# Performance work log

Measured on AMD Instinct MI355X. Metric: run time of the kernel, lower is better.

The kernel has to match this reference:

```python
import jax, jax.numpy as jnp
import numpy as np

B, S, DIM, H = 8, 1024, 1024, 16
D = DIM // H  # d_head = 64


def setup_inputs() -> dict:
    key = jax.random.key(0)
    ks = jax.random.split(key, 7)
    scale = 1.0 / np.sqrt(D)  # nn.Linear default init range ~ U(-1/sqrt(in), 1/sqrt(in))
    x = jax.random.normal(ks[0], (B, S, DIM), dtype=jnp.float32)
    Wq = jax.random.uniform(ks[1], (H, D, D), jnp.float32, -scale, scale)
    Wk = jax.random.uniform(ks[2], (H, D, D), jnp.float32, -scale, scale)
    Wv = jax.random.uniform(ks[3], (H, D, D), jnp.float32, -scale, scale)
    bq = jax.random.uniform(ks[4], (H, D), jnp.float32, -scale, scale)
    bk = jax.random.uniform(ks[5], (H, D), jnp.float32, -scale, scale)
    bv = jax.random.uniform(ks[6], (H, D), jnp.float32, -scale, scale)
    return {"x": x, "Wq": Wq, "Wk": Wk, "Wv": Wv, "bq": bq, "bk": bk, "bv": bv}


def reference(x, Wq, Wk, Wv, bq, bk, bv):
    # x: [B,S,DIM] -> split heads: [B,S,H,D] (matches per-head column slicing)
    xh = x.reshape(x.shape[0], x.shape[1], H, D)
    # per-head linear: y = x @ W.T + b  (nn.Linear convention: weight [out,in])
    q = jnp.einsum('bshd,hed->bshe', xh, Wq) + bq  # [B,S,H,D]
    k = jnp.einsum('bshd,hed->bshe', xh, Wk) + bk
    v = jnp.einsum('bshd,hed->bshe', xh, Wv) + bv
    scores = jnp.einsum('bqhd,bkhd->bhqk', q, k) / jnp.sqrt(jnp.float32(D))
    attn = jax.nn.softmax(scores, axis=-1)  # [B,H,S,S]
    out = jnp.einsum('bhqk,bkhd->bqhd', attn, v)  # [B,S,H,D]
    # hstack over heads == merge last two dims back to DIM
    return out.reshape(x.shape[0], x.shape[1], H * D)
```

## Files before the change

kernel.cpp:

```cpp
#include <hip/hip_runtime.h>
#include <hip/hip_bf16.h>

#define BB 8
#define SS 1024
#define HH 16
#define DD 64
#define DIMM 1024
#define NUNITS (BB * HH)
#define UNIT_ELEMS (SS * DD)

typedef __attribute__((ext_vector_type(8))) short short8;
typedef __attribute__((ext_vector_type(4))) float f32x4;

__device__ inline short f2b(float f) {
    __hip_bfloat16 h = __float2bfloat16(f);
    return *reinterpret_cast<short*>(&h);
}

__global__ __launch_bounds__(256) void qkv_proj(
    const float* __restrict__ x, const float* __restrict__ Wq,
    const float* __restrict__ Wk, const float* __restrict__ Wv,
    const float* __restrict__ bqp, const float* __restrict__ bkp,
    const float* __restrict__ bvp,
    short* __restrict__ Qo, short* __restrict__ Ko, short* __restrict__ Vto,
    int unit0)
{
    __shared__ alignas(16) short xs[64][72];
    __shared__ alignas(16) short wsm[3][64][72];
    __shared__ alignas(16) short tr[64][72];

    const int t = threadIdx.x;
    const int bid = blockIdx.x;
    const int st = bid & 15;
    const int ul = bid >> 4;
    const int unit = unit0 + ul;
    const int h = unit & 15;
    const int b = unit >> 4;
    const int s0 = st * 64;

    for (int i = 0; i < 4; ++i) {
        int g = t + i * 256;
        int r = g >> 4, c = (g & 15) * 4;
        float4 xv = *reinterpret_cast<const float4*>(
            x + ((size_t)(b * SS + s0 + r)) * DIMM + h * DD + c);
        short4 sv; sv.x = f2b(xv.x); sv.y = f2b(xv.y); sv.z = f2b(xv.z); sv.w = f2b(xv.w);
        *reinterpret_cast<short4*>(&xs[r][c]) = sv;
    }
    {
        const float* Wsrc[3] = {Wq + h * DD * DD, Wk + h * DD * DD, Wv + h * DD * DD};
        for (int m = 0; m < 3; ++m)
            for (int i = 0; i < 4; ++i) {
                int g = t + i * 256;
                int e = g >> 4, c = (g & 15) * 4;
                float4 wv = *reinterpret_cast<const float4*>(Wsrc[m] + e * DD + c);
                short4 sv; sv.x = f2b(wv.x); sv.y = f2b(wv.y); sv.z = f2b(wv.z); sv.w = f2b(wv.w);
                *reinterpret_cast<short4*>(&wsm[m][e][c]) = sv;
            }
    }
    __syncthreads();

    const int lane = t & 63, w = t >> 6;
    const int l15 = lane & 15, quad = lane >> 4;

    short8 a0 = *reinterpret_cast<const short8*>(&xs[w * 16 + l15][quad * 8]);
    short8 a1 = *reinterpret_cast<const short8*>(&xs[w * 16 + l15][32 + quad * 8]);

    const float* biases[3] = {bqp, bkp, bvp};

    for (int m = 0; m < 3; ++m) {
        for (int et = 0; et < 4; ++et) {
            short8 w0 = *reinterpret_cast<const short8*>(&wsm[m][et * 16 + l15][quad * 8]);
            short8 w1 = *reinterpret_cast<const short8*>(&wsm[m][et * 16 + l15][32 + quad * 8]);
            f32x4 acc = {0.f, 0.f, 0.f, 0.f};
            acc = __builtin_amdgcn_mfma_f32_16x16x32_bf16(a0, w0, acc, 0, 0, 0);
            acc = __builtin_amdgcn_mfma_f32_16x16x32_bf16(a1, w1, acc, 0, 0, 0);
            float bias = biases[m][h * DD + et * 16 + l15];
            for (int r = 0; r < 4; ++r) {
                float v = acc[r] + bias;
                int e = et * 16 + l15;
                int srow = w * 16 + quad * 4 + r;
                if (m == 0) {
                    tr[srow][e] = f2b(v * 0.125f);
                } else if (m == 1) {
                    tr[srow][e] = f2b(v);
                } else {
                    tr[e][srow] = f2b(v);
                }
            }
        }
        __syncthreads();
        for (int i = 0; i < 2; ++i) {
            int g = t + i * 256;
            int row = g >> 3, col = (g & 7) * 8;
            short8 val = *reinterpret_cast<const short8*>(&tr[row][col]);
            if (m == 0)
                *reinterpret_cast<short8*>(Qo + ((size_t)ul * SS + s0 + row) * DD + col) = val;
            else if (m == 1)
                *reinterpret_cast<short8*>(Ko + ((size_t)ul * SS + s0 + row) * DD + col) = val;
            else
                *reinterpret_cast<short8*>(Vto + ((size_t)ul * DD + row) * SS + s0 + col) = val;
        }
        __syncthreads();
    }
}

__global__ __launch_bounds__(256, 4) void attn(
    const short* __restrict__ Q, const short* __restrict__ K,
    const short* __restrict__ Vt, float* __restrict__ out, int unit0)
{
    __shared__ alignas(16) short ks[64][72];
    __shared__ alignas(16) short vts[64][72];
    __shared__ alignas(16) short ps[4][32][72];

    const int t = threadIdx.x;
    const int bid = blockIdx.x;
    const int qt = bid & 7;
    const int ul = bid >> 3;
    const int unit = unit0 + ul;
    const int h = unit & 15;
    const int b = unit >> 4;
    const int q0 = qt * 128;
    const int lane = t & 63, w = t >> 6;
    const int l15 = lane & 15, quad = lane >> 4;

    short8 qa[2][2];
    for (int s = 0; s < 2; ++s) {
        const short* qp = Q + ((size_t)ul * SS + q0 + s * 64 + w * 16 + l15) * DD;
        qa[s][0] = *reinterpret_cast<const short8*>(qp + quad * 8);
        qa[s][1] = *reinterpret_cast<const short8*>(qp + 32 + quad * 8);
    }

    short8 ones;
    for (int j = 0; j < 8; ++j) ones[j] = (short)0x3F80;

    f32x4 o[8];
    f32x4 lacc[2];
    for (int i = 0; i < 8; ++i) o[i] = (f32x4){0.f, 0.f, 0.f, 0.f};
    lacc[0] = (f32x4){0.f, 0.f, 0.f, 0.f};
    lacc[1] = (f32x4){0.f, 0.f, 0.f, 0.f};

    const int srow_ = t >> 3, scol = (t & 7) * 8;

    const float L2E = 1.44269504f;
    const float MBIAS = 11.5415603f;

    for (int kt = 0; kt < 16; ++kt) {
        const int k0 = kt * 64;
        __syncthreads();
        for (int i = 0; i < 2; ++i) {
            int row = srow_ + i * 32;
            *reinterpret_cast<short8*>(&ks[row][scol]) =
                *reinterpret_cast<const short8*>(K + ((size_t)ul * SS + k0 + row) * DD + scol);
            *reinterpret_cast<short8*>(&vts[row][scol]) =
                *reinterpret_cast<const short8*>(Vt + ((size_t)ul * DD + row) * SS + k0 + scol);
        }
        __syncthreads();

        for (int n = 0; n < 4; ++n) {
            short8 kb0 = *reinterpret_cast<const short8*>(&ks[n * 16 + l15][quad * 8]);
            short8 kb1 = *reinterpret_cast<const short8*>(&ks[n * 16 + l15][32 + quad * 8]);
            for (int s = 0; s < 2; ++s) {
                f32x4 acc = {0.f, 0.f, 0.f, 0.f};
                acc = __builtin_amdgcn_mfma_f32_16x16x32_bf16(qa[s][0], kb0, acc, 0, 0, 0);
                acc = __builtin_amdgcn_mfma_f32_16x16x32_bf16(qa[s][1], kb1, acc, 0, 0, 0);
                for (int r = 0; r < 4; ++r) {
                    float p = exp2f(fmaf(acc[r], L2E, -MBIAS));
                    ps[w][s * 16 + quad * 4 + r][n * 16 + l15] = f2b(p);
                }
            }
        }

        short8 pa[2][2];
        for (int s = 0; s < 2; ++s) {
            pa[s][0] = *reinterpret_cast<const short8*>(&ps[w][s * 16 + l15][quad * 8]);
            pa[s][1] = *reinterpret_cast<const short8*>(&ps[w][s * 16 + l15][32 + quad * 8]);
            lacc[s] = __builtin_amdgcn_mfma_f32_16x16x32_bf16(pa[s][0], ones, lacc[s], 0, 0, 0);
            lacc[s] = __builtin_amdgcn_mfma_f32_16x16x32_bf16(pa[s][1], ones, lacc[s], 0, 0, 0);
        }
        for (int dt = 0; dt < 4; ++dt) {
            short8 vb0 = *reinterpret_cast<const short8*>(&vts[dt * 16 + l15][quad * 8]);
            short8 vb1 = *reinterpret_cast<const short8*>(&vts[dt * 16 + l15][32 + quad * 8]);
            for (int s = 0; s < 2; ++s) {
                o[s * 4 + dt] = __builtin_amdgcn_mfma_f32_16x16x32_bf16(pa[s][0], vb0, o[s * 4 + dt], 0, 0, 0);
                o[s * 4 + dt] = __builtin_amdgcn_mfma_f32_16x16x32_bf16(pa[s][1], vb1, o[s * 4 + dt], 0, 0, 0);
            }
        }
    }

    for (int s = 0; s < 2; ++s)
        for (int dt = 0; dt < 4; ++dt)
            for (int r = 0; r < 4; ++r) {
                int srow = q0 + s * 64 + w * 16 + quad * 4 + r;
                int col = h * DD + dt * 16 + l15;
                out[((size_t)b * SS + srow) * DIMM + col] = o[s * 4 + dt][r] / lacc[s][r];
            }
}

extern "C" void kernel_launch(void* const* d_in, const int* in_sizes, int n_in,
                              void* d_out, int out_size, void* d_ws, size_t ws_size,
                              hipStream_t stream) {
    const float* x   = (const float*)d_in[0];
    const float* Wq  = (const float*)d_in[1];
    const float* Wk  = (const float*)d_in[2];
    const float* Wv  = (const float*)d_in[3];
    const float* bqp = (const float*)d_in[4];
    const float* bkp = (const float*)d_in[5];
    const float* bvp = (const float*)d_in[6];
    float* out = (float*)d_out;

    const size_t unit_bytes = 3ULL * UNIT_ELEMS * sizeof(short);
    int U = (int)(ws_size / unit_bytes);
    if (U < 1) U = 1;
    if (U > NUNITS) U = NUNITS;

    short* Qw  = (short*)d_ws;
    short* Kw  = Qw + (size_t)U * UNIT_ELEMS;
    short* Vtw = Kw + (size_t)U * UNIT_ELEMS;

    for (int u0 = 0; u0 < NUNITS; u0 += U) {
        int nu = NUNITS - u0 < U ? NUNITS - u0 : U;
        qkv_proj<<<dim3(nu * 16), dim3(256), 0, stream>>>(
            x, Wq, Wk, Wv, bqp, bkp, bvp, Qw, Kw, Vtw, u0);
        attn<<<dim3(nu * 8), dim3(256), 0, stream>>>(Qw, Kw, Vtw, out, u0);
    }
}
```

Baseline: 167.8 us.

## Pre-convert weights to bf16 once, shrink projection LDS, remap attention blocks

Adds a small kernel that converts all Q/K/V weights to bf16 once into workspace, so each projection block loads bf16 weights directly instead of reconverting fp32. The projection kernel now computes all twelve accumulator tiles first and reuses the weight LDS buffer for the transpose staging. That cuts shared memory and allows a 4-blocks-per-CU launch bound. The attention kernel remaps block indices when all units run in one launch, which changes how work is spread across XCDs and caches. It also swaps the bf16 conversion intrinsic for manual round-to-nearest-even bit math. The costs are an extra launch, extra workspace, and more live registers in the projection kernel.

```diff
diff --git a/kernel.cpp b/kernel.cpp
--- a/kernel.cpp
+++ b/kernel.cpp
@@ -8,26 +8,43 @@
 #define DIMM 1024
 #define NUNITS (BB * HH)
 #define UNIT_ELEMS (SS * DD)
+#define NW (3 * HH * DD * DD)
 
 typedef __attribute__((ext_vector_type(8))) short short8;
 typedef __attribute__((ext_vector_type(4))) float f32x4;
 
 __device__ inline short f2b(float f) {
-    __hip_bfloat16 h = __float2bfloat16(f);
-    return *reinterpret_cast<short*>(&h);
-}
-
-__global__ __launch_bounds__(256) void qkv_proj(
-    const float* __restrict__ x, const float* __restrict__ Wq,
-    const float* __restrict__ Wk, const float* __restrict__ Wv,
+    unsigned u = __float_as_uint(f);
+    u = (u + 0x7FFFu + ((u >> 16) & 1u)) >> 16;
+    return (short)u;
+}
+
+__global__ __launch_bounds__(256) void wconv(
+    const float* __restrict__ Wq, const float* __restrict__ Wk,
+    const float* __restrict__ Wv, short* __restrict__ Wb)
+{
+    int idx = (blockIdx.x * 256 + threadIdx.x) * 8;
+    if (idx >= NW) return;
+    int m = idx >> 16;
+    int r = idx & 65535;
+    const float* src = (m == 0) ? Wq : (m == 1) ? Wk : Wv;
+    float4 a = *reinterpret_cast<const float4*>(src + r);
+    float4 b = *reinterpret_cast<const float4*>(src + r + 4);
+    short8 o;
+    o[0] = f2b(a.x); o[1] = f2b(a.y); o[2] = f2b(a.z); o[3] = f2b(a.w);
+    o[4] = f2b(b.x); o[5] = f2b(b.y); o[6] = f2b(b.z); o[7] = f2b(b.w);
+    *reinterpret_cast<short8*>(Wb + idx) = o;
+}
+
+__global__ __launch_bounds__(256, 4) void qkv_proj(
+    const float* __restrict__ x, const short* __restrict__ Wb,
     const float* __restrict__ bqp, const float* __restrict__ bkp,
     const float* __restrict__ bvp,
     short* __restrict__ Qo, short* __restrict__ Ko, short* __restrict__ Vto,
     int unit0)
 {
+    __shared__ alignas(16) short wsm[3][64][72];
     __shared__ alignas(16) short xs[64][72];
-    __shared__ alignas(16) short wsm[3][64][72];
-    __shared__ alignas(16) short tr[64][72];
 
     const int t = threadIdx.x;
     const int bid = blockIdx.x;
@@ -38,6 +55,13 @@
     const int b = unit >> 4;
     const int s0 = st * 64;
 
+    for (int m = 0; m < 3; ++m)
+        for (int i = 0; i < 2; ++i) {
+            int g = t + i * 256;
+            int row = g >> 3, col = (g & 7) * 8;
+            *reinterpret_cast<short8*>(&wsm[m][row][col]) =
+                *reinterpret_cast<const short8*>(Wb + ((size_t)(m * HH + h)) * 4096 + row * 64 + col);
+        }
     for (int i = 0; i < 4; ++i) {
         int g = t + i * 256;
         int r = g >> 4, c = (g & 15) * 4;
@@ -46,17 +70,6 @@
         short4 sv; sv.x = f2b(xv.x); sv.y = f2b(xv.y); sv.z = f2b(xv.z); sv.w = f2b(xv.w);
         *reinterpret_cast<short4*>(&xs[r][c]) = sv;
     }
-    {
-        const float* Wsrc[3] = {Wq + h * DD * DD, Wk + h * DD * DD, Wv + h * DD * DD};
-        for (int m = 0; m < 3; ++m)
-            for (int i = 0; i < 4; ++i) {
-                int g = t + i * 256;
-                int e = g >> 4, c = (g & 15) * 4;
-                float4 wv = *reinterpret_cast<const float4*>(Wsrc[m] + e * DD + c);
-                short4 sv; sv.x = f2b(wv.x); sv.y = f2b(wv.y); sv.z = f2b(wv.z); sv.w = f2b(wv.w);
-                *reinterpret_cast<short4*>(&wsm[m][e][c]) = sv;
-            }
-    }
     __syncthreads();
 
     const int lane = t & 63, w = t >> 6;
@@ -65,34 +78,38 @@
     short8 a0 = *reinterpret_cast<const short8*>(&xs[w * 16 + l15][quad * 8]);
     short8 a1 = *reinterpret_cast<const short8*>(&xs[w * 16 + l15][32 + quad * 8]);
 
-    const float* biases[3] = {bqp, bkp, bvp};
-
-    for (int m = 0; m < 3; ++m) {
+    f32x4 acc[12];
+    for (int m = 0; m < 3; ++m)
         for (int et = 0; et < 4; ++et) {
             short8 w0 = *reinterpret_cast<const short8*>(&wsm[m][et * 16 + l15][quad * 8]);
             short8 w1 = *reinterpret_cast<const short8*>(&wsm[m][et * 16 + l15][32 + quad * 8]);
-            f32x4 acc = {0.f, 0.f, 0.f, 0.f};
-            acc = __builtin_amdgcn_mfma_f32_16x16x32_bf16(a0, w0, acc, 0, 0, 0);
-            acc = __builtin_amdgcn_mfma_f32_16x16x32_bf16(a1, w1, acc, 0, 0, 0);
+            f32x4 a = {0.f, 0.f, 0.f, 0.f};
+            a = __builtin_amdgcn_mfma_f32_16x16x32_bf16(a0, w0, a, 0, 0, 0);
+            a = __builtin_amdgcn_mfma_f32_16x16x32_bf16(a1, w1, a, 0, 0, 0);
+            acc[m * 4 + et] = a;
+        }
+    __syncthreads();
+
+    const float* biases[3] = {bqp, bkp, bvp};
+    for (int m = 0; m < 3; ++m)
+        for (int et = 0; et < 4; ++et) {
             float bias = biases[m][h * DD + et * 16 + l15];
+            int e = et * 16 + l15;
             for (int r = 0; r < 4; ++r) {
-                float v = acc[r] + bias;
-                int e = et * 16 + l15;
+                float v = acc[m * 4 + et][r] + bias;
                 int srow = w * 16 + quad * 4 + r;
-                if (m == 0) {
-                    tr[srow][e] = f2b(v * 0.125f);
-                } else if (m == 1) {
-                    tr[srow][e] = f2b(v);
-                } else {
-                    tr[e][srow] = f2b(v);
-                }
-            }
-        }
-        __syncthreads();
+                if (m == 0)      wsm[0][srow][e] = f2b(v * 0.125f);
+                else if (m == 1) wsm[1][srow][e] = f2b(v);
+                else             wsm[2][e][srow] = f2b(v);
+            }
+        }
+    __syncthreads();
+
+    for (int m = 0; m < 3; ++m)
         for (int i = 0; i < 2; ++i) {
             int g = t + i * 256;
             int row = g >> 3, col = (g & 7) * 8;
-            short8 val = *reinterpret_cast<const short8*>(&tr[row][col]);
+            short8 val = *reinterpret_cast<const short8*>(&wsm[m][row][col]);
             if (m == 0)
                 *reinterpret_cast<short8*>(Qo + ((size_t)ul * SS + s0 + row) * DD + col) = val;
             else if (m == 1)
@@ -100,13 +117,11 @@
             else
                 *reinterpret_cast<short8*>(Vto + ((size_t)ul * DD + row) * SS + s0 + col) = val;
         }
-        __syncthreads();
-    }
 }
 
 __global__ __launch_bounds__(256, 4) void attn(
     const short* __restrict__ Q, const short* __restrict__ K,
-    const short* __restrict__ Vt, float* __restrict__ out, int unit0)
+    const short* __restrict__ Vt, float* __restrict__ out, int unit0, int nu)
 {
     __shared__ alignas(16) short ks[64][72];
     __shared__ alignas(16) short vts[64][72];
@@ -114,8 +129,16 @@
 
     const int t = threadIdx.x;
     const int bid = blockIdx.x;
-    const int qt = bid & 7;
-    const int ul = bid >> 3;
+    int ul, qt;
+    if (nu == NUNITS) {
+        int xslot = bid & 7;
+        int j = bid >> 3;
+        ul = xslot * 16 + (j & 15);
+        qt = j >> 4;
+    } else {
+        ul = bid >> 3;
+        qt = bid & 7;
+    }
     const int unit = unit0 + ul;
     const int h = unit & 15;
     const int b = unit >> 4;
@@ -160,11 +183,11 @@
             short8 kb0 = *reinterpret_cast<const short8*>(&ks[n * 16 + l15][quad * 8]);
             short8 kb1 = *reinterpret_cast<const short8*>(&ks[n * 16 + l15][32 + quad * 8]);
             for (int s = 0; s < 2; ++s) {
-                f32x4 acc = {0.f, 0.f, 0.f, 0.f};
-                acc = __builtin_amdgcn_mfma_f32_16x16x32_bf16(qa[s][0], kb0, acc, 0, 0, 0);
-                acc = __builtin_amdgcn_mfma_f32_16x16x32_bf16(qa[s][1], kb1, acc, 0, 0, 0);
+                f32x4 a = {0.f, 0.f, 0.f, 0.f};
+                a = __builtin_amdgcn_mfma_f32_16x16x32_bf16(qa[s][0], kb0, a, 0, 0, 0);
+                a = __builtin_amdgcn_mfma_f32_16x16x32_bf16(qa[s][1], kb1, a, 0, 0, 0);
                 for (int r = 0; r < 4; ++r) {
-                    float p = exp2f(fmaf(acc[r], L2E, -MBIAS));
+                    float p = exp2f(fmaf(a[r], L2E, -MBIAS));
                     ps[w][s * 16 + quad * 4 + r][n * 16 + l15] = f2b(p);
                 }
             }
@@ -208,19 +231,24 @@
     const float* bvp = (const float*)d_in[6];
     float* out = (float*)d_out;
 
+    short* Wb = (short*)d_ws;
+    const size_t w_elems = NW;
     const size_t unit_bytes = 3ULL * UNIT_ELEMS * sizeof(short);
-    int U = (int)(ws_size / unit_bytes);
+    size_t avail = ws_size > w_elems * 2 ? ws_size - w_elems * 2 : 0;
+    int U = (int)(avail / unit_bytes);
     if (U < 1) U = 1;
     if (U > NUNITS) U = NUNITS;
 
-    short* Qw  = (short*)d_ws;
+    short* Qw  = Wb + w_elems;
     short* Kw  = Qw + (size_t)U * UNIT_ELEMS;
     short* Vtw = Kw + (size_t)U * UNIT_ELEMS;
+
+    wconv<<<dim3((NW / 8 + 255) / 256), dim3(256), 0, stream>>>(Wq, Wk, Wv, Wb);
 
     for (int u0 = 0; u0 < NUNITS; u0 += U) {
         int nu = NUNITS - u0 < U ? NUNITS - u0 : U;
         qkv_proj<<<dim3(nu * 16), dim3(256), 0, stream>>>(
-            x, Wq, Wk, Wv, bqp, bkp, bvp, Qw, Kw, Vtw, u0);
-        attn<<<dim3(nu * 8), dim3(256), 0, stream>>>(Qw, Kw, Vtw, out, u0);
-    }
-}
+            x, Wb, bqp, bkp, bvp, Qw, Kw, Vtw, u0);
+        attn<<<dim3(nu * 8), dim3(256), 0, stream>>>(Qw, Kw, Vtw, out, u0, nu);
+    }
+}
```

Result: slower. 173.7 us (+3.5%).
